# Kernel optimization log

Measured on AMD Instinct MI355X. Metric: run time of the kernel, lower is better.

## Reference

```python
import jax, jax.numpy as jnp
import numpy as np

C, N, E, G = 8, 50000, 800000, 64
HID, HL, OL = 128, 2, 2
EPS = 1e-5


def sh_l012(vec):
    """e3nn real spherical harmonics l=0,1,2, normalize=True, component normalization. [E,3]->[E,9]"""
    r = jnp.sqrt(jnp.sum(vec * vec, axis=-1, keepdims=True) + 1e-12)
    u = vec / r
    x, y, z = u[:, 0], u[:, 1], u[:, 2]
    s3, s15, s5 = jnp.sqrt(3.0), jnp.sqrt(15.0), jnp.sqrt(5.0)
    y0 = jnp.ones_like(x)[:, None]
    y1 = s3 * u
    y2 = jnp.stack([s15 * x * z, s15 * x * y, s5 * (y * y - 0.5 * (x * x + z * z)),
                    s15 * y * z, 0.5 * s15 * (z * z - x * x)], axis=-1)
    return jnp.concatenate([y0, y1, y2], axis=-1)


def norm_act(s, v, d):
    """e3nn NormActivation(relu, eps): x * relu(n)/n per irrep instance."""
    ns = jnp.sqrt(s * s + EPS * EPS)
    nv = jnp.sqrt(jnp.sum(v * v, -1, keepdims=True) + EPS * EPS)
    nd = jnp.sqrt(jnp.sum(d * d, -1, keepdims=True) + EPS * EPS)
    return s * (jax.nn.relu(ns) / ns), v * (jax.nn.relu(nv) / nv), d * (jax.nn.relu(nd) / nd)


def o3_linear(s, v, d, W0, W1, W2):
    """o3.Linear: mixes multiplicities per l independently."""
    return s @ W0, jnp.einsum('nim,ic->ncm', v, W1), jnp.einsum('nim,ic->ncm', d, W2)


def tf_update(s, v, d, W0, W1, W2, Wd, edge_src, edge_dst):
    """Equivariant transformer update. W0/W1/W2 stacked [3(q,k,v), Cin, C], Wd [3(l), C, C]."""
    qs, qv, qd = norm_act(*o3_linear(s, v, d, W0[0], W1[0], W2[0]))
    ks, kv, kd = norm_act(*o3_linear(s, v, d, W0[1], W1[1], W2[1]))
    vs, vv, vd = norm_act(*o3_linear(s, v, d, W0[2], W1[2], W2[2]))
    # FullyConnectedTensorProduct(q,k)->0e: per-l channel-pair weighted inner products
    logit = (jnp.einsum('ec,ed,cd->e', qs[edge_dst], ks[edge_src], Wd[0])
             + jnp.einsum('ecm,edm,cd->e', qv[edge_dst], kv[edge_src], Wd[1]) / jnp.sqrt(3.0)
             + jnp.einsum('ecm,edm,cd->e', qd[edge_dst], kd[edge_src], Wd[2]) / jnp.sqrt(5.0))
    expv = jnp.exp(logit)
    z = jax.ops.segment_sum(expv, edge_dst, num_segments=N)
    z = jnp.where(z == 0, 1.0, z)
    w = jnp.sqrt(jax.nn.relu(expv / z[edge_dst]))  # relu(alpha).sqrt()
    os = jax.ops.segment_sum(w[:, None] * vs[edge_src], edge_dst, num_segments=N)
    ov = jax.ops.segment_sum(w[:, None, None] * vv[edge_src], edge_dst, num_segments=N)
    od = jax.ops.segment_sum(w[:, None, None] * vd[edge_src], edge_dst, num_segments=N)
    return os, ov, od


def setup_inputs() -> dict:
    key = jax.random.key(0)
    ks = jax.random.split(key, 20)
    inp = {}
    inp['x_scalars'] = jax.random.normal(ks[0], (N, 9), jnp.float32)
    inp['edge_vec'] = jax.random.normal(ks[1], (E, 3), jnp.float32)
    inp['et0_W0'] = jax.random.normal(ks[2], (3, 10, C), jnp.float32) / jnp.sqrt(10.0)
    inp['et0_W1'] = jax.random.normal(ks[3], (3, 1, C), jnp.float32)
    inp['et0_W2'] = jax.random.normal(ks[4], (3, 1, C), jnp.float32)
    inp['et0_Wd'] = jax.random.normal(ks[5], (3, C, C), jnp.float32) / C
    inp['h_W0'] = jax.random.normal(ks[6], (HL, 3, C, C), jnp.float32) / jnp.sqrt(float(C))
    inp['h_W1'] = jax.random.normal(ks[7], (HL, 3, C, C), jnp.float32) / jnp.sqrt(float(C))
    inp['h_W2'] = jax.random.normal(ks[8], (HL, 3, C, C), jnp.float32) / jnp.sqrt(float(C))
    inp['h_Wd'] = jax.random.normal(ks[9], (HL, 3, C, C), jnp.float32) / C
    inp['Wol'] = jax.random.normal(ks[10], (C, HID), jnp.float32) / jnp.sqrt(float(C))
    inp['Wlin'] = jax.random.normal(ks[11], (OL, HID, HID), jnp.float32) / jnp.sqrt(float(HID))
    inp['blin'] = jax.random.normal(ks[12], (OL, HID), jnp.float32) * 0.01
    inp['Wout'] = jax.random.normal(ks[13], (HID, 9), jnp.float32) / jnp.sqrt(float(HID))
    inp['bout'] = jax.random.normal(ks[14], (9,), jnp.float32) * 0.01
    inp['edge_src'] = jax.random.randint(ks[15], (E,), 0, N, jnp.int32)
    inp['edge_dst'] = jax.random.randint(ks[16], (E,), 0, N, jnp.int32)
    inp['batch_seg'] = jnp.sort(jax.random.randint(ks[17], (N,), 0, G, jnp.int32))
    return inp


def reference(x_scalars, edge_vec, et0_W0, et0_W1, et0_W2, et0_Wd,
              h_W0, h_W1, h_W2, h_Wd, Wol, Wlin, blin, Wout, bout,
              edge_src, edge_dst, batch_seg):
    sh = sh_l012(edge_vec)  # [E,9]
    cnt = jnp.maximum(jax.ops.segment_sum(jnp.ones((E,), sh.dtype), edge_dst, num_segments=N), 1.0)
    node_sh = jax.ops.segment_sum(sh, edge_dst, num_segments=N) / cnt[:, None]  # [N,9]
    s = jnp.concatenate([x_scalars, node_sh[:, :1]], axis=1)  # [N,10] 0e
    v = node_sh[:, 1:4][:, None, :]   # [N,1,3] 1e
    d = node_sh[:, 4:9][:, None, :]   # [N,1,5] 2e
    s, v, d = tf_update(s, v, d, et0_W0, et0_W1, et0_W2, et0_Wd, edge_src, edge_dst)
    for l in range(HL):
        hs, hv, hd = tf_update(s, v, d, h_W0[l], h_W1[l], h_W2[l], h_Wd[l], edge_src, edge_dst)
        s, v, d = s + hs, v + hv, d + hd
    # ol: irreps_output -> hidden x 0e (only scalar part maps to scalars)
    h = s @ Wol
    h = h / jnp.maximum(jnp.sqrt(jnp.sum(h * h, 1, keepdims=True)), 1e-12)  # F.normalize
    h = jax.nn.relu(h)
    for i in range(OL):
        h = jax.nn.relu(h @ Wlin[i] + blin[i])
    seg = batch_seg[edge_src]
    cg = jnp.maximum(jax.ops.segment_sum(jnp.ones((E,), h.dtype), seg, num_segments=G), 1.0)
    m = jax.ops.segment_sum(h[edge_src], seg, num_segments=G) / cg[:, None]
    return jax.nn.softmax(m @ Wout + bout, axis=1)
```

## Files before the change

kernel.cpp:

```cpp
#include <hip/hip_runtime.h>
#include <hip/hip_fp16.h>
#include <math.h>

#define NN 50000
#define NE 800000
#define NG 64
#define QH 80
#define KVH 144

__global__ void k_count(const int* __restrict__ esrc, const int* __restrict__ edst,
                        int* __restrict__ indeg, int* __restrict__ outdeg, int E)
{
  int e = blockIdx.x*blockDim.x + threadIdx.x;
  if (e >= E) return;
  atomicAdd(indeg + edst[e], 1);
  atomicAdd(outdeg + esrc[e], 1);
}

__global__ void __launch_bounds__(256) k_scan1(const int* __restrict__ indeg,
                                               int* __restrict__ bsum, int N)
{
  __shared__ int sh[256];
  int t = threadIdx.x;
  int lo = blockIdx.x*2048 + t*8;
  int s = 0;
  #pragma unroll
  for (int k = 0; k < 8; ++k) {
    int i = lo + k;
    if (i < N) s += indeg[i];
  }
  sh[t] = s;
  __syncthreads();
  for (int off = 128; off > 0; off >>= 1) {
    if (t < off) sh[t] += sh[t+off];
    __syncthreads();
  }
  if (t == 0) bsum[blockIdx.x] = sh[0];
}

__global__ void k_scan2(int* __restrict__ bsum, int nb)
{
  if (threadIdx.x == 0) {
    int run = 0;
    for (int i = 0; i < nb; ++i) { int x = bsum[i]; bsum[i] = run; run += x; }
  }
}

__global__ void __launch_bounds__(256) k_scan3(const int* __restrict__ indeg,
                                               const int* __restrict__ bsum,
                                               int* __restrict__ rowptr, int N)
{
  __shared__ int sh[256];
  int t = threadIdx.x;
  int lo = blockIdx.x*2048 + t*8;
  int v[8];
  int s = 0;
  #pragma unroll
  for (int k = 0; k < 8; ++k) {
    int i = lo + k;
    v[k] = (i < N) ? indeg[i] : 0;
    s += v[k];
  }
  sh[t] = s;
  __syncthreads();
  for (int off = 1; off < 256; off <<= 1) {
    int x = 0;
    if (t >= off) x = sh[t-off];
    __syncthreads();
    if (t >= off) sh[t] += x;
    __syncthreads();
  }
  int run = bsum[blockIdx.x] + (t > 0 ? sh[t-1] : 0);
  #pragma unroll
  for (int k = 0; k < 8; ++k) {
    int i = lo + k;
    if (i < N) rowptr[i] = run;
    if (i == N-1) rowptr[N] = run + v[k];
    run += v[k];
  }
}

__global__ void k_fill(const int* __restrict__ esrc, const int* __restrict__ edst,
                       const int* __restrict__ rowptr, int* __restrict__ cursor,
                       int2* __restrict__ csr, int E)
{
  int e = blockIdx.x*blockDim.x + threadIdx.x;
  if (e >= E) return;
  int d = edst[e];
  int slot = rowptr[d] + atomicAdd(cursor + d, 1);
  csr[slot] = make_int2(esrc[e], e);
}

template<int CS, int CV, bool INIT>
__global__ void __launch_bounds__(256) k_node_feats(
    const float* __restrict__ in,
    const float* __restrict__ evec,
    const int2* __restrict__ csr,
    const int* __restrict__ rowptr,
    const float* __restrict__ W0,
    const float* __restrict__ W1,
    const float* __restrict__ W2,
    const float* __restrict__ Wd,
    __half* __restrict__ qt,
    __half* __restrict__ kv,
    int N)
{
  int n = blockIdx.x*blockDim.x + threadIdx.x;
  if (n >= N) return;
  float s_in[CS];
  float v_in[CV][3];
  float d_in[CV][5];

  if constexpr (INIT) {
    int b = rowptr[n], e2 = rowptr[n+1];
    float acc[9];
    #pragma unroll
    for (int j = 0; j < 9; ++j) acc[j] = 0.f;
    const float s3  = 1.7320508075688772f;
    const float s15 = 3.872983346207417f;
    const float s5  = 2.23606797749979f;
    for (int s = b; s < e2; ++s) {
      int eid = csr[s].y;
      float vx = evec[3*eid+0], vy = evec[3*eid+1], vz = evec[3*eid+2];
      float r = sqrtf(vx*vx + vy*vy + vz*vz + 1e-12f);
      float x = vx / r, y = vy / r, z = vz / r;
      acc[0] += 1.f;
      acc[1] += s3*x; acc[2] += s3*y; acc[3] += s3*z;
      acc[4] += s15*x*z;
      acc[5] += s15*x*y;
      acc[6] += s5*(y*y - 0.5f*(x*x + z*z));
      acc[7] += s15*y*z;
      acc[8] += 0.5f*s15*(z*z - x*x);
    }
    int dg = e2 - b;
    float inv = 1.f / (float)(dg > 1 ? dg : 1);
    #pragma unroll
    for (int j = 0; j < 9; ++j) s_in[j] = in[(size_t)n*9 + j];
    s_in[9] = acc[0]*inv;
    #pragma unroll
    for (int m = 0; m < 3; ++m) v_in[0][m] = acc[1+m]*inv;
    #pragma unroll
    for (int m = 0; m < 5; ++m) d_in[0][m] = acc[4+m]*inv;
  } else {
    const float* x = in + (size_t)n*72;
    #pragma unroll
    for (int i = 0; i < CS; ++i) s_in[i] = x[i];
    #pragma unroll
    for (int i = 0; i < CV; ++i)
      #pragma unroll
      for (int m = 0; m < 3; ++m) v_in[i][m] = x[CS + i*3 + m];
    #pragma unroll
    for (int i = 0; i < CV; ++i)
      #pragma unroll
      for (int m = 0; m < 5; ++m) d_in[i][m] = x[CS + 3*CV + i*5 + m];
  }

  const float inv_s3 = 0.5773502691896258f;
  const float inv_s5 = 0.4472135954999579f;

  #pragma unroll
  for (int t = 0; t < 3; ++t) {
    float ss[8];
    float vv[8][3];
    float dd[8][5];
    #pragma unroll
    for (int c = 0; c < 8; ++c) {
      float a = 0.f;
      #pragma unroll
      for (int i = 0; i < CS; ++i) a += s_in[i]*W0[t*CS*8 + i*8 + c];
      ss[c] = a;
    }
    #pragma unroll
    for (int c = 0; c < 8; ++c)
      #pragma unroll
      for (int m = 0; m < 3; ++m) {
        float a = 0.f;
        #pragma unroll
        for (int i = 0; i < CV; ++i) a += v_in[i][m]*W1[t*CV*8 + i*8 + c];
        vv[c][m] = a;
      }
    #pragma unroll
    for (int c = 0; c < 8; ++c)
      #pragma unroll
      for (int m = 0; m < 5; ++m) {
        float a = 0.f;
        #pragma unroll
        for (int i = 0; i < CV; ++i) a += d_in[i][m]*W2[t*CV*8 + i*8 + c];
        dd[c][m] = a;
      }

    if (t == 0) {
      __half* q = qt + (size_t)n*QH;
      #pragma unroll
      for (int dp = 0; dp < 8; ++dp) {
        float a = 0.f;
        #pragma unroll
        for (int c = 0; c < 8; ++c) a += ss[c]*Wd[0*64 + c*8 + dp];
        q[dp] = __float2half(a);
      }
      #pragma unroll
      for (int dp = 0; dp < 8; ++dp)
        #pragma unroll
        for (int m = 0; m < 3; ++m) {
          float a = 0.f;
          #pragma unroll
          for (int c = 0; c < 8; ++c) a += vv[c][m]*Wd[1*64 + c*8 + dp];
          q[8 + dp*3 + m] = __float2half(a*inv_s3);
        }
      #pragma unroll
      for (int dp = 0; dp < 8; ++dp)
        #pragma unroll
        for (int m = 0; m < 5; ++m) {
          float a = 0.f;
          #pragma unroll
          for (int c = 0; c < 8; ++c) a += dd[c][m]*Wd[2*64 + c*8 + dp];
          q[32 + dp*5 + m] = __float2half(a*inv_s5);
        }
    } else {
      __half* o = kv + (size_t)n*KVH + (t == 1 ? 0 : 72);
      #pragma unroll
      for (int c = 0; c < 8; ++c) o[c] = __float2half(ss[c]);
      #pragma unroll
      for (int c = 0; c < 8; ++c)
        #pragma unroll
        for (int m = 0; m < 3; ++m) o[8 + c*3 + m] = __float2half(vv[c][m]);
      #pragma unroll
      for (int c = 0; c < 8; ++c)
        #pragma unroll
        for (int m = 0; m < 5; ++m) o[32 + c*5 + m] = __float2half(dd[c][m]);
    }
  }
}

#define AT2_NPB 8
__global__ void __launch_bounds__(256) k_attn2(
    const __half* __restrict__ qt,
    const __half* __restrict__ kv,
    const int2* __restrict__ csr,
    const int* __restrict__ rowptr,
    const float* __restrict__ base,
    float* __restrict__ out, int N)
{
  typedef _Float16 h2 __attribute__((ext_vector_type(2)));
  const float LOG2E_HALF = 0.7213475204444817f;

  int t = threadIdx.x;
  int hw = t >> 5, lane = t & 31;
  int n = blockIdx.x*AT2_NPB + hw;
  if (n >= N) return;

  uint4 qraw = make_uint4(0,0,0,0);
  if (lane < 9)
    qraw = *(const uint4*)((const char*)qt + (size_t)n*(QH*2) + (size_t)lane*16);
  h2 qh0 = __builtin_bit_cast(h2, qraw.x);
  h2 qh1 = __builtin_bit_cast(h2, qraw.y);
  h2 qh2 = __builtin_bit_cast(h2, qraw.z);
  h2 qh3 = __builtin_bit_cast(h2, qraw.w);

  int b = rowptr[n], e2 = rowptr[n+1];
  float Z = 0.f;
  float A[8];
  #pragma unroll
  for (int i = 0; i < 8; ++i) A[i] = 0.f;

  const char* kvb = (const char*)kv;

  auto dot8 = [&](uint4 raw) -> float {
    float d = 0.f;
#if __has_builtin(__builtin_amdgcn_fdot2)
    d = __builtin_amdgcn_fdot2(qh0, __builtin_bit_cast(h2, raw.x), d, false);
    d = __builtin_amdgcn_fdot2(qh1, __builtin_bit_cast(h2, raw.y), d, false);
    d = __builtin_amdgcn_fdot2(qh2, __builtin_bit_cast(h2, raw.z), d, false);
    d = __builtin_amdgcn_fdot2(qh3, __builtin_bit_cast(h2, raw.w), d, false);
#else
    const __half* qp = (const __half*)&qraw;
    const __half* kp = (const __half*)&raw;
    #pragma unroll
    for (int i = 0; i < 8; ++i)
      d += __half2float(qp[i]) * __half2float(kp[i]);
#endif
    return d;
  };

  int s = b;
  for (; s + 4 <= e2; s += 4) {
    uint4 raw0 = make_uint4(0,0,0,0), raw1 = raw0, raw2 = raw0, raw3 = raw0;
    int src0 = csr[s].x, src1 = csr[s+1].x, src2 = csr[s+2].x, src3 = csr[s+3].x;
    if (lane < 18) {
      raw0 = *(const uint4*)(kvb + (size_t)src0*(KVH*2) + (size_t)lane*16);
      raw1 = *(const uint4*)(kvb + (size_t)src1*(KVH*2) + (size_t)lane*16);
      raw2 = *(const uint4*)(kvb + (size_t)src2*(KVH*2) + (size_t)lane*16);
      raw3 = *(const uint4*)(kvb + (size_t)src3*(KVH*2) + (size_t)lane*16);
    }
    float d0 = dot8(raw0), d1 = dot8(raw1), d2 = dot8(raw2), d3 = dot8(raw3);
    #pragma unroll
    for (int off = 1; off < 32; off <<= 1) {
      d0 += __shfl_xor(d0, off, 32);
      d1 += __shfl_xor(d1, off, 32);
      d2 += __shfl_xor(d2, off, 32);
      d3 += __shfl_xor(d3, off, 32);
    }
    float e0 = exp2f(LOG2E_HALF*d0);
    float e1 = exp2f(LOG2E_HALF*d1);
    float e2v = exp2f(LOG2E_HALF*d2);
    float e3 = exp2f(LOG2E_HALF*d3);
    Z += e0*e0 + e1*e1 + e2v*e2v + e3*e3;
    const __half* h0 = (const __half*)&raw0;
    const __half* h1 = (const __half*)&raw1;
    const __half* h2p = (const __half*)&raw2;
    const __half* h3 = (const __half*)&raw3;
    #pragma unroll
    for (int i = 0; i < 8; ++i)
      A[i] += e0*__half2float(h0[i]) + e1*__half2float(h1[i])
            + e2v*__half2float(h2p[i]) + e3*__half2float(h3[i]);
  }
  for (; s < e2; ++s) {
    uint4 raw0 = make_uint4(0,0,0,0);
    int src0 = csr[s].x;
    if (lane < 18)
      raw0 = *(const uint4*)(kvb + (size_t)src0*(KVH*2) + (size_t)lane*16);
    float d0 = dot8(raw0);
    #pragma unroll
    for (int off = 1; off < 32; off <<= 1) d0 += __shfl_xor(d0, off, 32);
    float e0 = exp2f(LOG2E_HALF*d0);
    Z += e0*e0;
    const __half* h0 = (const __half*)&raw0;
    #pragma unroll
    for (int i = 0; i < 8; ++i) A[i] += e0*__half2float(h0[i]);
  }

  float rz = (Z > 0.f) ? rsqrtf(Z) : 0.f;
  if (lane >= 9 && lane < 18) {
    int o0 = (lane - 9)*8;
    float r[8];
    #pragma unroll
    for (int i = 0; i < 8; ++i) r[i] = A[i]*rz;
    float* op = out + (size_t)n*72 + o0;
    if (base) {
      const float* bp = base + (size_t)n*72 + o0;
      #pragma unroll
      for (int i = 0; i < 8; ++i) r[i] += bp[i];
    }
    *(float4*)op     = make_float4(r[0], r[1], r[2], r[3]);
    *(float4*)(op+4) = make_float4(r[4], r[5], r[6], r[7]);
  }
}

#define HD_NODES 64
__global__ void __launch_bounds__(512) k_head(
    const float* __restrict__ svd,
    const float* __restrict__ Wol,
    const float* __restrict__ Wlin,
    const float* __restrict__ blin,
    const int* __restrict__ outdeg,
    const int* __restrict__ bseg,
    float* __restrict__ m,
    float* __restrict__ cg,
    int N)
{
  __shared__ float hs[HD_NODES][128];
  __shared__ float Ws[64][128];
  __shared__ float ssm[HD_NODES][8];
  __shared__ float nrm_p[HD_NODES][33];
  __shared__ float rinv[HD_NODES];
  int t = threadIdx.x;
  int n0 = blockIdx.x*HD_NODES;
  int tc = t & 31, tr = t >> 5;
  int c0 = tc*4;
  int nb = tr*4;

  {
    int node = t >> 3, i = t & 7;
    int gn = n0 + node;
    ssm[node][i] = (gn < N) ? svd[(size_t)gn*72 + i] : 0.f;
  }
  __syncthreads();

  float acc[4][4];
  #pragma unroll
  for (int nd = 0; nd < 4; ++nd)
    #pragma unroll
    for (int cc = 0; cc < 4; ++cc) acc[nd][cc] = 0.f;
  #pragma unroll
  for (int i = 0; i < 8; ++i) {
    float4 wv = *(const float4*)(Wol + i*128 + c0);
    #pragma unroll
    for (int nd = 0; nd < 4; ++nd) {
      float a = ssm[nb+nd][i];
      acc[nd][0] += a*wv.x; acc[nd][1] += a*wv.y;
      acc[nd][2] += a*wv.z; acc[nd][3] += a*wv.w;
    }
  }
  #pragma unroll
  for (int nd = 0; nd < 4; ++nd) {
    *(float4*)&hs[nb+nd][c0] = make_float4(acc[nd][0],acc[nd][1],acc[nd][2],acc[nd][3]);
    nrm_p[nb+nd][tc] = acc[nd][0]*acc[nd][0] + acc[nd][1]*acc[nd][1]
                     + acc[nd][2]*acc[nd][2] + acc[nd][3]*acc[nd][3];
  }
  __syncthreads();
  if (t < HD_NODES) {
    float sq = 0.f;
    #pragma unroll
    for (int k = 0; k < 32; ++k) sq += nrm_p[t][k];
    rinv[t] = 1.f / fmaxf(sqrtf(sq), 1e-12f);
  }
  __syncthreads();
  #pragma unroll
  for (int k = 0; k < 16; ++k) {
    int idx = t + k*512;
    int node = idx >> 7, c = idx & 127;
    hs[node][c] = fmaxf(hs[node][c]*rinv[node], 0.f);
  }

  for (int l = 0; l < 2; ++l) {
    float4 bv = *(const float4*)(blin + l*128 + c0);
    float a2[4][4];
    #pragma unroll
    for (int nd = 0; nd < 4; ++nd) {
      a2[nd][0]=bv.x; a2[nd][1]=bv.y; a2[nd][2]=bv.z; a2[nd][3]=bv.w;
    }
    #pragma unroll
    for (int hhalf = 0; hhalf < 2; ++hhalf) {
      __syncthreads();
      {
        const float4* src = (const float4*)(Wlin + l*16384 + hhalf*64*128);
        float4* dst = (float4*)&Ws[0][0];
        #pragma unroll
        for (int k = 0; k < 4; ++k) dst[t + k*512] = src[t + k*512];
      }
      __syncthreads();
      int r0 = hhalf*64;
      for (int i = 0; i < 64; i += 4) {
        float av[4][4];
        #pragma unroll
        for (int nd = 0; nd < 4; ++nd)
          *(float4*)av[nd] = *(const float4*)&hs[nb+nd][r0 + i];
        #pragma unroll
        for (int ii = 0; ii < 4; ++ii) {
          float4 wv = *(const float4*)&Ws[i+ii][c0];
          #pragma unroll
          for (int nd = 0; nd < 4; ++nd) {
            a2[nd][0] += av[nd][ii]*wv.x;
            a2[nd][1] += av[nd][ii]*wv.y;
            a2[nd][2] += av[nd][ii]*wv.z;
            a2[nd][3] += av[nd][ii]*wv.w;
          }
        }
      }
    }
    __syncthreads();
    #pragma unroll
    for (int nd = 0; nd < 4; ++nd)
      *(float4*)&hs[nb+nd][c0] = make_float4(
          fmaxf(a2[nd][0],0.f), fmaxf(a2[nd][1],0.f),
          fmaxf(a2[nd][2],0.f), fmaxf(a2[nd][3],0.f));
  }
  __syncthreads();

  if (t < 128) {
    int c = t;
    float accm = 0.f; int gprev = -1;
    for (int nn = 0; nn < HD_NODES; ++nn) {
      int n = n0 + nn;
      if (n >= N) break;
      int g = bseg[n];
      if (g != gprev) {
        if (gprev >= 0) atomicAdd(&m[gprev*128 + c], accm);
        accm = 0.f; gprev = g;
      }
      accm += (float)outdeg[n]*hs[nn][c];
    }
    if (gprev >= 0) atomicAdd(&m[gprev*128 + c], accm);
  } else if (t == 128) {
    float a = 0.f; int gp = -1;
    for (int nn = 0; nn < HD_NODES; ++nn) {
      int n = n0 + nn;
      if (n >= N) break;
      int g = bseg[n];
      if (g != gp) {
        if (gp >= 0) atomicAdd(&cg[gp], a);
        a = 0.f; gp = g;
      }
      a += (float)outdeg[n];
    }
    if (gp >= 0) atomicAdd(&cg[gp], a);
  }
}

__global__ void k_out(const float* __restrict__ m, const float* __restrict__ cg,
                      const float* __restrict__ Wout, const float* __restrict__ bout,
                      float* __restrict__ out)
{
  int g = threadIdx.x;
  if (g >= NG) return;
  float inv = 1.f / fmaxf(cg[g], 1.f);
  float v[9];
  #pragma unroll
  for (int j = 0; j < 9; ++j) {
    float a = 0.f;
    for (int i = 0; i < 128; ++i) a += m[g*128 + i]*Wout[i*9 + j];
    v[j] = a*inv + bout[j];
  }
  float mxv = v[0];
  #pragma unroll
  for (int j = 1; j < 9; ++j) mxv = fmaxf(mxv, v[j]);
  float sum = 0.f;
  #pragma unroll
  for (int j = 0; j < 9; ++j) { v[j] = expf(v[j] - mxv); sum += v[j]; }
  #pragma unroll
  for (int j = 0; j < 9; ++j) out[g*9 + j] = v[j]/sum;
}

extern "C" void kernel_launch(void* const* d_in, const int* in_sizes, int n_in,
                              void* d_out, int out_size, void* d_ws, size_t ws_size,
                              hipStream_t stream) {
  (void)in_sizes; (void)n_in; (void)out_size; (void)ws_size;
  const float* x_scalars = (const float*)d_in[0];
  const float* edge_vec  = (const float*)d_in[1];
  const float* et0_W0    = (const float*)d_in[2];
  const float* et0_W1    = (const float*)d_in[3];
  const float* et0_W2    = (const float*)d_in[4];
  const float* et0_Wd    = (const float*)d_in[5];
  const float* h_W0      = (const float*)d_in[6];
  const float* h_W1      = (const float*)d_in[7];
  const float* h_W2      = (const float*)d_in[8];
  const float* h_Wd      = (const float*)d_in[9];
  const float* Wol       = (const float*)d_in[10];
  const float* Wlin      = (const float*)d_in[11];
  const float* blin      = (const float*)d_in[12];
  const float* Wout      = (const float*)d_in[13];
  const float* bout      = (const float*)d_in[14];
  const int*   esrc      = (const int*)d_in[15];
  const int*   edst      = (const int*)d_in[16];
  const int*   bseg      = (const int*)d_in[17];

  const int N = NN, E = NE;

  char* w = (char*)d_ws;
  auto alloc = [&](size_t nbytes) {
    char* p = w;
    w += (nbytes + 255) & ~(size_t)255;
    return p;
  };
  int*    deg3   = (int*)   alloc((size_t)3*N*4);
  int*    indeg  = deg3;
  int*    outdeg = deg3 + N;
  int*    cursor = deg3 + 2*N;
  int*    rowptr = (int*)   alloc((size_t)(N+1)*4);
  int*    bsum   = (int*)   alloc((size_t)32*4);
  int2*   csr    = (int2*)  alloc((size_t)E*8);
  float*  stA    = (float*) alloc((size_t)N*72*4);
  float*  stB    = (float*) alloc((size_t)N*72*4);
  __half* qt     = (__half*)alloc((size_t)N*QH*2);
  __half* kv     = (__half*)alloc((size_t)N*KVH*2);
  float*  pool   = (float*) alloc((size_t)(NG*128 + NG)*4);
  float*  mpool  = pool;
  float*  cgp    = pool + NG*128;

  hipMemsetAsync(deg3, 0, (size_t)3*N*4, stream);
  hipMemsetAsync(pool, 0, (size_t)(NG*128 + NG)*4, stream);

  const int TB = 256;
  const int gE  = (E + TB - 1) / TB;
  const int gN  = (N + TB - 1) / TB;
  const int gA2 = (N + AT2_NPB - 1) / AT2_NPB;
  const int gHD = (N + HD_NODES - 1) / HD_NODES;
  const int gSC = (N + 2047) / 2048;

  k_count<<<gE, TB, 0, stream>>>(esrc, edst, indeg, outdeg, E);
  k_scan1<<<gSC, 256, 0, stream>>>(indeg, bsum, N);
  k_scan2<<<1, 64, 0, stream>>>(bsum, gSC);
  k_scan3<<<gSC, 256, 0, stream>>>(indeg, bsum, rowptr, N);
  k_fill<<<gE, TB, 0, stream>>>(esrc, edst, rowptr, cursor, csr, E);

  k_node_feats<10,1,true><<<gN, TB, 0, stream>>>(
      x_scalars, edge_vec, csr, rowptr,
      et0_W0, et0_W1, et0_W2, et0_Wd, qt, kv, N);
  k_attn2<<<gA2, 256, 0, stream>>>(qt, kv, csr, rowptr, nullptr, stA, N);

  float* cur = stA; float* oth = stB;
  for (int l = 0; l < 2; ++l) {
    k_node_feats<8,8,false><<<gN, TB, 0, stream>>>(
        cur, nullptr, nullptr, nullptr,
        h_W0 + l*192, h_W1 + l*192, h_W2 + l*192, h_Wd + l*192, qt, kv, N);
    k_attn2<<<gA2, 256, 0, stream>>>(qt, kv, csr, rowptr, cur, oth, N);
    float* t = cur; cur = oth; oth = t;
  }

  k_head<<<gHD, 512, 0, stream>>>(cur, Wol, Wlin, blin, outdeg, bseg, mpool, cgp, N);
  k_out<<<1, 64, 0, stream>>>(mpool, cgp, Wout, bout, (float*)d_out);
}
```

Before: 448.0 us.

## Unroll attention gather to 8 edges, vectorize node loads, slim head LDS

Result: slower. 493.1 us (+10.1%).

```diff
diff --git a/kernel.cpp b/kernel.cpp
--- a/kernel.cpp
+++ b/kernel.cpp
@@ -142,17 +142,20 @@
     #pragma unroll
     for (int m = 0; m < 5; ++m) d_in[0][m] = acc[4+m]*inv;
   } else {
-    const float* x = in + (size_t)n*72;
-    #pragma unroll
-    for (int i = 0; i < CS; ++i) s_in[i] = x[i];
+    float xf[72];
+    const float4* xr = (const float4*)(in + (size_t)n*72);
+    #pragma unroll
+    for (int k = 0; k < 18; ++k) *(float4*)&xf[k*4] = xr[k];
+    #pragma unroll
+    for (int i = 0; i < CS; ++i) s_in[i] = xf[i];
     #pragma unroll
     for (int i = 0; i < CV; ++i)
       #pragma unroll
-      for (int m = 0; m < 3; ++m) v_in[i][m] = x[CS + i*3 + m];
+      for (int m = 0; m < 3; ++m) v_in[i][m] = xf[CS + i*3 + m];
     #pragma unroll
     for (int i = 0; i < CV; ++i)
       #pragma unroll
-      for (int m = 0; m < 5; ++m) d_in[i][m] = x[CS + 3*CV + i*5 + m];
+      for (int m = 0; m < 5; ++m) d_in[i][m] = xf[CS + 3*CV + i*5 + m];
   }
 
   const float inv_s3 = 0.5773502691896258f;
@@ -264,6 +267,8 @@
   for (int i = 0; i < 8; ++i) A[i] = 0.f;
 
   const char* kvb = (const char*)kv;
+  const bool ld = (lane < 18);
+  const size_t loff = (size_t)lane*16;
 
   auto dot8 = [&](uint4 raw) -> float {
     float d = 0.f;
@@ -283,42 +288,65 @@
   };
 
   int s = b;
-  for (; s + 4 <= e2; s += 4) {
-    uint4 raw0 = make_uint4(0,0,0,0), raw1 = raw0, raw2 = raw0, raw3 = raw0;
-    int src0 = csr[s].x, src1 = csr[s+1].x, src2 = csr[s+2].x, src3 = csr[s+3].x;
-    if (lane < 18) {
-      raw0 = *(const uint4*)(kvb + (size_t)src0*(KVH*2) + (size_t)lane*16);
-      raw1 = *(const uint4*)(kvb + (size_t)src1*(KVH*2) + (size_t)lane*16);
-      raw2 = *(const uint4*)(kvb + (size_t)src2*(KVH*2) + (size_t)lane*16);
-      raw3 = *(const uint4*)(kvb + (size_t)src3*(KVH*2) + (size_t)lane*16);
-    }
-    float d0 = dot8(raw0), d1 = dot8(raw1), d2 = dot8(raw2), d3 = dot8(raw3);
+  for (; s + 8 <= e2; s += 8) {
+    uint4 raw[8];
+    #pragma unroll
+    for (int u = 0; u < 8; ++u) {
+      int src = csr[s+u].x;
+      raw[u] = make_uint4(0,0,0,0);
+      if (ld) raw[u] = *(const uint4*)(kvb + (size_t)src*(KVH*2) + loff);
+    }
+    float d[8];
+    #pragma unroll
+    for (int u = 0; u < 8; ++u) d[u] = dot8(raw[u]);
     #pragma unroll
     for (int off = 1; off < 32; off <<= 1) {
-      d0 += __shfl_xor(d0, off, 32);
-      d1 += __shfl_xor(d1, off, 32);
-      d2 += __shfl_xor(d2, off, 32);
-      d3 += __shfl_xor(d3, off, 32);
-    }
-    float e0 = exp2f(LOG2E_HALF*d0);
-    float e1 = exp2f(LOG2E_HALF*d1);
-    float e2v = exp2f(LOG2E_HALF*d2);
-    float e3 = exp2f(LOG2E_HALF*d3);
-    Z += e0*e0 + e1*e1 + e2v*e2v + e3*e3;
-    const __half* h0 = (const __half*)&raw0;
-    const __half* h1 = (const __half*)&raw1;
-    const __half* h2p = (const __half*)&raw2;
-    const __half* h3 = (const __half*)&raw3;
-    #pragma unroll
-    for (int i = 0; i < 8; ++i)
-      A[i] += e0*__half2float(h0[i]) + e1*__half2float(h1[i])
-            + e2v*__half2float(h2p[i]) + e3*__half2float(h3[i]);
+      #pragma unroll
+      for (int u = 0; u < 8; ++u) d[u] += __shfl_xor(d[u], off, 32);
+    }
+    float e[8];
+    #pragma unroll
+    for (int u = 0; u < 8; ++u) {
+      e[u] = exp2f(LOG2E_HALF*d[u]);
+      Z += e[u]*e[u];
+    }
+    #pragma unroll
+    for (int u = 0; u < 8; ++u) {
+      const __half* h = (const __half*)&raw[u];
+      #pragma unroll
+      for (int i = 0; i < 8; ++i) A[i] += e[u]*__half2float(h[i]);
+    }
+  }
+  if (s + 4 <= e2) {
+    uint4 raw[4];
+    #pragma unroll
+    for (int u = 0; u < 4; ++u) {
+      int src = csr[s+u].x;
+      raw[u] = make_uint4(0,0,0,0);
+      if (ld) raw[u] = *(const uint4*)(kvb + (size_t)src*(KVH*2) + loff);
+    }
+    float d[4];
+    #pragma unroll
+    for (int u = 0; u < 4; ++u) d[u] = dot8(raw[u]);
+    #pragma unroll
+    for (int off = 1; off < 32; off <<= 1) {
+      #pragma unroll
+      for (int u = 0; u < 4; ++u) d[u] += __shfl_xor(d[u], off, 32);
+    }
+    #pragma unroll
+    for (int u = 0; u < 4; ++u) {
+      float e = exp2f(LOG2E_HALF*d[u]);
+      Z += e*e;
+      const __half* h = (const __half*)&raw[u];
+      #pragma unroll
+      for (int i = 0; i < 8; ++i) A[i] += e*__half2float(h[i]);
+    }
+    s += 4;
   }
   for (; s < e2; ++s) {
     uint4 raw0 = make_uint4(0,0,0,0);
     int src0 = csr[s].x;
-    if (lane < 18)
-      raw0 = *(const uint4*)(kvb + (size_t)src0*(KVH*2) + (size_t)lane*16);
+    if (ld) raw0 = *(const uint4*)(kvb + (size_t)src0*(KVH*2) + loff);
     float d0 = dot8(raw0);
     #pragma unroll
     for (int off = 1; off < 32; off <<= 1) d0 += __shfl_xor(d0, off, 32);
@@ -359,10 +387,8 @@
     int N)
 {
   __shared__ float hs[HD_NODES][128];
-  __shared__ float Ws[64][128];
+  __shared__ float Ws[32][128];
   __shared__ float ssm[HD_NODES][8];
-  __shared__ float nrm_p[HD_NODES][33];
-  __shared__ float rinv[HD_NODES];
   int t = threadIdx.x;
   int n0 = blockIdx.x*HD_NODES;
   int tc = t & 31, tr = t >> 5;
@@ -393,23 +419,14 @@
   }
   #pragma unroll
   for (int nd = 0; nd < 4; ++nd) {
-    *(float4*)&hs[nb+nd][c0] = make_float4(acc[nd][0],acc[nd][1],acc[nd][2],acc[nd][3]);
-    nrm_p[nb+nd][tc] = acc[nd][0]*acc[nd][0] + acc[nd][1]*acc[nd][1]
-                     + acc[nd][2]*acc[nd][2] + acc[nd][3]*acc[nd][3];
-  }
-  __syncthreads();
-  if (t < HD_NODES) {
-    float sq = 0.f;
-    #pragma unroll
-    for (int k = 0; k < 32; ++k) sq += nrm_p[t][k];
-    rinv[t] = 1.f / fmaxf(sqrtf(sq), 1e-12f);
-  }
-  __syncthreads();
-  #pragma unroll
-  for (int k = 0; k < 16; ++k) {
-    int idx = t + k*512;
-    int node = idx >> 7, c = idx & 127;
-    hs[node][c] = fmaxf(hs[node][c]*rinv[node], 0.f);
+    float p = acc[nd][0]*acc[nd][0] + acc[nd][1]*acc[nd][1]
+            + acc[nd][2]*acc[nd][2] + acc[nd][3]*acc[nd][3];
+    #pragma unroll
+    for (int off = 1; off < 32; off <<= 1) p += __shfl_xor(p, off, 32);
+    float rinv = 1.f / fmaxf(sqrtf(p), 1e-12f);
+    *(float4*)&hs[nb+nd][c0] = make_float4(
+        fmaxf(acc[nd][0]*rinv, 0.f), fmaxf(acc[nd][1]*rinv, 0.f),
+        fmaxf(acc[nd][2]*rinv, 0.f), fmaxf(acc[nd][3]*rinv, 0.f));
   }
 
   for (int l = 0; l < 2; ++l) {
@@ -420,17 +437,17 @@
       a2[nd][0]=bv.x; a2[nd][1]=bv.y; a2[nd][2]=bv.z; a2[nd][3]=bv.w;
     }
     #pragma unroll
-    for (int hhalf = 0; hhalf < 2; ++hhalf) {
+    for (int q = 0; q < 4; ++q) {
       __syncthreads();
       {
-        const float4* src = (const float4*)(Wlin + l*16384 + hhalf*64*128);
+        const float4* src = (const float4*)(Wlin + l*16384 + q*4096);
         float4* dst = (float4*)&Ws[0][0];
-        #pragma unroll
-        for (int k = 0; k < 4; ++k) dst[t + k*512] = src[t + k*512];
+        dst[t] = src[t];
+        dst[t + 512] = src[t + 512];
       }
       __syncthreads();
-      int r0 = hhalf*64;
-      for (int i = 0; i < 64; i += 4) {
+      int r0 = q*32;
+      for (int i = 0; i < 32; i += 4) {
         float av[4][4];
         #pragma unroll
         for (int nd = 0; nd < 4; ++nd)
```
